# Kernel tuning notes

Measured on AMD Instinct MI355X. Metric: run time of the kernel, lower is better.

Reference implementation:

```python
import jax, jax.numpy as jnp
import numpy as np

B, T, IDIM = 16, 1024, 345
L, D, H, DK, FF = 4, 256, 4, 64, 1024
EPS = 1e-5


def layer_norm(x, s, b):
    m = jnp.mean(x, axis=-1, keepdims=True)
    v = jnp.mean(jnp.square(x - m), axis=-1, keepdims=True)
    return (x - m) * jax.lax.rsqrt(v + EPS) * s + b


def setup_inputs() -> dict:
    key = jax.random.key(0)
    ks = jax.random.split(key, 16)
    w = 0.02
    return {
        "x": jax.random.normal(ks[0], (B, T, IDIM), jnp.float32),
        "num_frames": int(T),
        "Win": w * jax.random.normal(ks[1], (IDIM, D), jnp.float32),
        "b_in": jnp.zeros((D,), jnp.float32),
        "ln1_s": jnp.ones((L, D), jnp.float32),
        "ln1_b": jnp.zeros((L, D), jnp.float32),
        "Wq": w * jax.random.normal(ks[2], (L, D, D), jnp.float32),
        "bq": jnp.zeros((L, D), jnp.float32),
        "Wk": w * jax.random.normal(ks[3], (L, D, D), jnp.float32),
        "bk": jnp.zeros((L, D), jnp.float32),
        "Wv": w * jax.random.normal(ks[4], (L, D, D), jnp.float32),
        "bv": jnp.zeros((L, D), jnp.float32),
        "Wo": w * jax.random.normal(ks[5], (L, D, D), jnp.float32),
        "bo": jnp.zeros((L, D), jnp.float32),
        "ln2_s": jnp.ones((L, D), jnp.float32),
        "ln2_b": jnp.zeros((L, D), jnp.float32),
        "W1": w * jax.random.normal(ks[6], (L, D, FF), jnp.float32),
        "b1": jnp.zeros((L, FF), jnp.float32),
        "W2": w * jax.random.normal(ks[7], (L, FF, D), jnp.float32),
        "b2": jnp.zeros((L, D), jnp.float32),
        "lno_s": jnp.ones((D,), jnp.float32),
        "lno_b": jnp.zeros((D,), jnp.float32),
    }


def reference(x, num_frames, Win, b_in, ln1_s, ln1_b, Wq, bq, Wk, bk, Wv, bv,
              Wo, bo, ln2_s, ln2_b, W1, b1, W2, b2, lno_s, lno_b):
    num = x.shape[0]
    scale = 1.0 / np.sqrt(DK)
    # [num*T, D]
    e = x.reshape(-1, x.shape[-1]) @ Win + b_in
    for i in range(L):
        e = layer_norm(e, ln1_s[i], ln1_b[i])
        # naive MHSA (residual taken from LN output, as in the source)
        q = (e @ Wq[i] + bq[i]).reshape(num, -1, H, DK)
        k = (e @ Wk[i] + bk[i]).reshape(num, -1, H, DK)
        v = (e @ Wv[i] + bv[i]).reshape(num, -1, H, DK)
        scores = jnp.einsum('bqhd,bkhd->bhqk', q, k) * scale
        attn = jax.nn.softmax(scores, axis=-1)
        o = jnp.einsum('bhqk,bkhd->bqhd', attn, v).reshape(-1, D)
        e = e + (o @ Wo[i] + bo[i])
        e = layer_norm(e, ln2_s[i], ln2_b[i])
        e = e + (jax.nn.relu(e @ W1[i] + b1[i]) @ W2[i] + b2[i])
    out = layer_norm(e, lno_s, lno_b)
    return out.reshape(num, num_frames, -1)
```

## Files before the change

kernel.cpp:

```cpp
#include <hip/hip_runtime.h>
#include <hip/hip_bf16.h>

#define BB    16
#define TT    1024
#define MTOK  (BB*TT)
#define IDIM_ 345
#define KPAD  384
#define LL    4
#define DD_   256
#define FF_   1024
#define EPS_  1e-5f
#define QSCL  0.18033688f
#define MSHIFT 12.0f

typedef __bf16 bf16;
typedef bf16 bf16x8 __attribute__((ext_vector_type(8)));
typedef float f32x4 __attribute__((ext_vector_type(4)));

static __device__ __forceinline__ f32x4 MFMA(bf16x8 a, bf16x8 b, f32x4 c) {
  return __builtin_amdgcn_mfma_f32_16x16x32_bf16(a, b, c, 0, 0, 0);
}
static __device__ __forceinline__ unsigned bfbits(float x) {
  return (unsigned)__builtin_bit_cast(unsigned short, (bf16)x);
}
static __device__ __forceinline__ bf16x8 ld_bf8(const void* p) {
  return *reinterpret_cast<const bf16x8*>(p);
}
static __device__ __forceinline__ void gload_lds16(const bf16* g, void* l) {
  __builtin_amdgcn_global_load_lds(
      (const __attribute__((address_space(1))) void*)g,
      (__attribute__((address_space(3))) void*)l, 16, 0, 0);
}

__global__ void k_convert_pad(const float* __restrict__ src, bf16* __restrict__ dst) {
  int idx = blockIdx.x * 256 + threadIdx.x;
  if (idx >= MTOK * (KPAD / 4)) return;
  int r = idx / (KPAD / 4), c0 = (idx % (KPAD / 4)) * 4;
  const float* s = src + (long)r * IDIM_ + c0;
  float v0 = (c0 + 0 < IDIM_) ? s[0] : 0.f;
  float v1 = (c0 + 1 < IDIM_) ? s[1] : 0.f;
  float v2 = (c0 + 2 < IDIM_) ? s[2] : 0.f;
  float v3 = (c0 + 3 < IDIM_) ? s[3] : 0.f;
  uint2 pk;
  pk.x = bfbits(v0) | (bfbits(v1) << 16);
  pk.y = bfbits(v2) | (bfbits(v3) << 16);
  *reinterpret_cast<uint2*>(dst + (long)r * KPAD + c0) = pk;
}

__global__ void k_wt_convert(const float* __restrict__ src, bf16* __restrict__ dst,
                             int K, int N, int Kp) {
  int idx = blockIdx.x * 256 + threadIdx.x;
  if (idx >= N * Kp) return;
  int n = idx / Kp, kk = idx % Kp;
  dst[idx] = (kk < K) ? (bf16)src[(long)kk * N + n] : (bf16)0.f;
}

__global__ __launch_bounds__(256)
void k_wt_all(const float* __restrict__ Wq, const float* __restrict__ Wk,
              const float* __restrict__ Wv, const float* __restrict__ Wo,
              const float* __restrict__ W1, const float* __restrict__ W2,
              bf16* __restrict__ Wqkvt, bf16* __restrict__ Wot,
              bf16* __restrict__ W1t, bf16* __restrict__ W2t) {
  __shared__ float tile[64][65];
  const int s = blockIdx.y, m = s >> 2, i = s & 3;
  const float* src; bf16* dst; int K, N;
  switch (m) {
    case 0: src = Wq + (long)i*65536;  dst = Wqkvt + (long)i*196608;          K=256;  N=256;  break;
    case 1: src = Wk + (long)i*65536;  dst = Wqkvt + (long)i*196608 + 65536;  K=256;  N=256;  break;
    case 2: src = Wv + (long)i*65536;  dst = Wqkvt + (long)i*196608 + 131072; K=256;  N=256;  break;
    case 3: src = Wo + (long)i*65536;  dst = Wot + (long)i*65536;             K=256;  N=256;  break;
    case 4: src = W1 + (long)i*262144; dst = W1t + (long)i*262144;            K=256;  N=1024; break;
    default:src = W2 + (long)i*262144; dst = W2t + (long)i*262144;            K=1024; N=256;  break;
  }
  const int tiles_n = N >> 6, ntiles = (K >> 6) * tiles_n;
  if (blockIdx.x >= ntiles) return;
  const int tk = blockIdx.x / tiles_n, tn = blockIdx.x % tiles_n;
  const int t = threadIdx.x, rq = t >> 6, cl = t & 63;
  #pragma unroll
  for (int i2 = 0; i2 < 16; i2++)
    tile[rq * 16 + i2][cl] = src[(long)(tk * 64 + rq * 16 + i2) * N + tn * 64 + cl];
  __syncthreads();
  #pragma unroll
  for (int i2 = 0; i2 < 16; i2++)
    dst[(long)(tn * 64 + rq * 16 + i2) * K + tk * 64 + cl] = (bf16)tile[cl][rq * 16 + i2];
}

__global__ void k_bias_concat(const float* __restrict__ bq, const float* __restrict__ bk,
                              const float* __restrict__ bv, float* __restrict__ bqkv) {
  int idx = blockIdx.x * 256 + threadIdx.x;
  if (idx >= LL * 768) return;
  int i = idx / 768, j = idx % 768;
  float v = (j < 256) ? bq[i*256 + j] : (j < 512 ? bk[i*256 + j - 256] : bv[i*256 + j - 512]);
  bqkv[idx] = v;
}

template<int EPI>
__global__ __launch_bounds__(512, 4)
void k_gemm_row(const bf16* __restrict__ A, const bf16* __restrict__ Wt,
                const float* __restrict__ bias, const bf16* __restrict__ resid,
                const float* __restrict__ lns, const float* __restrict__ lnb,
                void* __restrict__ out, int K) {
  __shared__ alignas(16) char As[4096];
  __shared__ alignas(16) char Bs[32768];
  __shared__ alignas(16) float redS[32][4];
  __shared__ alignas(16) float redQ[32][4];
  const int t = threadIdx.x, lane = t & 63, wid = t >> 6;
  const int wr = wid >> 2, wc = wid & 3;
  const int g = lane >> 4, c = lane & 15;
  int flat = blockIdx.x;
  flat = (flat & 7) * 64 + (flat >> 3);
  const int mbase = flat * 32;

  const int srow = t >> 3;
  const int slot = ((t & 7) ^ (srow & 7)) * 8;
  const bf16* ag = A  + (long)(mbase + srow) * K + slot;
  const bf16* bg = Wt + (long)srow * K + slot;
  const int swz = (c & 7) << 4;

  f32x4 acc[4] = {};

  const int nk = K >> 6;
  for (int kt = 0; kt < nk; ++kt) {
    const int k0 = kt * 64;
    __syncthreads();
    if (wid < 4) gload_lds16(ag + k0, As + wid * 1024);
    #pragma unroll
    for (int p = 0; p < 4; p++)
      gload_lds16(bg + (long)(p * 64) * K + k0, Bs + p * 8192 + wid * 1024);
    __syncthreads();

    bf16x8 af[2], bfr[4][2];
    #pragma unroll
    for (int ks = 0; ks < 2; ks++)
      af[ks] = ld_bf8(As + (wr * 16 + c) * 128 + ((ks * 64 + g * 16) ^ swz));
    #pragma unroll
    for (int ni = 0; ni < 4; ni++)
      #pragma unroll
      for (int ks = 0; ks < 2; ks++)
        bfr[ni][ks] = ld_bf8(Bs + (wc * 64 + ni * 16 + c) * 128 + ((ks * 64 + g * 16) ^ swz));
    __builtin_amdgcn_s_setprio(1);
    #pragma unroll
    for (int ni = 0; ni < 4; ni++)
      #pragma unroll
      for (int ks = 0; ks < 2; ks++)
        acc[ni] = MFMA(af[ks], bfr[ni][ks], acc[ni]);
    __builtin_amdgcn_s_setprio(0);
  }

  float v[4][4];
  float sP[4] = {0.f, 0.f, 0.f, 0.f}, qP[4] = {0.f, 0.f, 0.f, 0.f};
  #pragma unroll
  for (int ni = 0; ni < 4; ni++) {
    const int col = wc * 64 + ni * 16 + c;
    const float bb = bias[col];
    #pragma unroll
    for (int j = 0; j < 4; j++) {
      const int row = mbase + wr * 16 + g * 4 + j;
      float r = resid ? (float)resid[(long)row * 256 + col] : 0.f;
      float x = acc[ni][j] + bb + r;
      v[ni][j] = x;
      sP[j] += x;
      qP[j] += x * x;
    }
  }
  #pragma unroll
  for (int j = 0; j < 4; j++) {
    #pragma unroll
    for (int off = 1; off < 16; off <<= 1) {
      sP[j] += __shfl_xor(sP[j], off);
      qP[j] += __shfl_xor(qP[j], off);
    }
  }
  if (c == 0) {
    #pragma unroll
    for (int j = 0; j < 4; j++) {
      const int rb = wr * 16 + g * 4 + j;
      redS[rb][wc] = sP[j];
      redQ[rb][wc] = qP[j];
    }
  }
  __syncthreads();

  #pragma unroll
  for (int j = 0; j < 4; j++) {
    const int rb = wr * 16 + g * 4 + j;
    const float4 s4 = *reinterpret_cast<const float4*>(redS[rb]);
    const float4 q4 = *reinterpret_cast<const float4*>(redQ[rb]);
    const float mean = (s4.x + s4.y + s4.z + s4.w) * (1.f / 256.f);
    const float var = (q4.x + q4.y + q4.z + q4.w) * (1.f / 256.f) - mean * mean;
    const float rstd = rsqrtf(var + EPS_);
    const long row = mbase + wr * 16 + g * 4 + j;
    #pragma unroll
    for (int ni = 0; ni < 4; ni++) {
      const int col = wc * 64 + ni * 16 + c;
      const float y = (v[ni][j] - mean) * rstd * lns[col] + lnb[col];
      if constexpr (EPI == 0) {
        ((bf16*)out)[row * 256 + col] = (bf16)y;
      } else {
        ((float*)out)[row * 256 + col] = y;
      }
    }
  }
}

template<int EPI>
__global__ __launch_bounds__(512, 4)
void k_ffn(const bf16* __restrict__ e, const bf16* __restrict__ W1t,
           const float* __restrict__ b1, const bf16* __restrict__ W2t,
           const float* __restrict__ b2, const float* __restrict__ lns,
           const float* __restrict__ lnb, void* __restrict__ out) {
  __shared__ alignas(16) char Ae[16384];
  __shared__ alignas(16) char Hs[16384];
  __shared__ alignas(16) char Bs[32768];
  __shared__ alignas(16) float redS[32][4];
  __shared__ alignas(16) float redQ[32][4];
  const int t = threadIdx.x, lane = t & 63, wid = t >> 6;
  const int wr = wid >> 2, wc = wid & 3;
  const int g = lane >> 4, c = lane & 15;
  int flat = blockIdx.x;
  flat = (flat & 7) * 64 + (flat >> 3);
  const int mbase = flat * 32;
  const int swz = (c & 7) << 4;

  #pragma unroll
  for (int p = 0; p < 2; p++) {
    const int ch = p * 512 + t;
    const int row = ch >> 5, s = ch & 31;
    const int srcb = (s >> 3) * 128 + (((s & 7) ^ (row & 7)) << 4);
    gload_lds16(e + (long)(mbase + row) * 256 + (srcb >> 1),
                Ae + p * 8192 + wid * 1024);
  }

  const int srow = t >> 3;
  const int slot = ((t & 7) ^ (srow & 7)) * 8;
  const int arow = wr * 16 + c;
  const int axo = (arow & 7) << 4;

  f32x4 acc2[4] = {};
  asm volatile("s_waitcnt vmcnt(0)" ::: "memory");
  __builtin_amdgcn_s_barrier();

  #pragma unroll 1
  for (int q = 0; q < 4; q++) {
    f32x4 acc1[4] = {};
    const bf16* bg1 = W1t + (long)(q * 256 + srow) * 256 + slot;
    for (int kt = 0; kt < 4; ++kt) {
      __syncthreads();
      #pragma unroll
      for (int p = 0; p < 4; p++)
        gload_lds16(bg1 + (long)(p * 64) * 256 + kt * 64, Bs + p * 8192 + wid * 1024);
      __syncthreads();
      bf16x8 af[2], bfr[4][2];
      #pragma unroll
      for (int ks = 0; ks < 2; ks++)
        af[ks] = ld_bf8(Ae + arow * 512 + ((kt * 128 + ks * 64 + g * 16) ^ axo));
      #pragma unroll
      for (int ni = 0; ni < 4; ni++)
        #pragma unroll
        for (int ks = 0; ks < 2; ks++)
          bfr[ni][ks] = ld_bf8(Bs + (wc * 64 + ni * 16 + c) * 128 + ((ks * 64 + g * 16) ^ swz));
      __builtin_amdgcn_s_setprio(1);
      #pragma unroll
      for (int ni = 0; ni < 4; ni++)
        #pragma unroll
        for (int ks = 0; ks < 2; ks++)
          acc1[ni] = MFMA(af[ks], bfr[ni][ks], acc1[ni]);
      __builtin_amdgcn_s_setprio(0);
    }
    #pragma unroll
    for (int ni = 0; ni < 4; ni++) {
      const int col = wc * 64 + ni * 16 + c;
      const float bb = b1[q * 256 + col];
      #pragma unroll
      for (int j = 0; j < 4; j++) {
        const int row = wr * 16 + g * 4 + j;
        *(bf16*)(Hs + row * 512 + ((col * 2) ^ ((row & 7) << 4))) =
            (bf16)fmaxf(acc1[ni][j] + bb, 0.f);
      }
    }
    __syncthreads();
    const bf16* bg2 = W2t + (long)srow * 1024 + q * 256 + slot;
    for (int kt = 0; kt < 4; ++kt) {
      __syncthreads();
      #pragma unroll
      for (int p = 0; p < 4; p++)
        gload_lds16(bg2 + (long)(p * 64) * 1024 + kt * 64, Bs + p * 8192 + wid * 1024);
      __syncthreads();
      bf16x8 af[2], bfr[4][2];
      #pragma unroll
      for (int ks = 0; ks < 2; ks++)
        af[ks] = ld_bf8(Hs + arow * 512 + ((kt * 128 + ks * 64 + g * 16) ^ axo));
      #pragma unroll
      for (int ni = 0; ni < 4; ni++)
        #pragma unroll
        for (int ks = 0; ks < 2; ks++)
          bfr[ni][ks] = ld_bf8(Bs + (wc * 64 + ni * 16 + c) * 128 + ((ks * 64 + g * 16) ^ swz));
      __builtin_amdgcn_s_setprio(1);
      #pragma unroll
      for (int ni = 0; ni < 4; ni++)
        #pragma unroll
        for (int ks = 0; ks < 2; ks++)
          acc2[ni] = MFMA(af[ks], bfr[ni][ks], acc2[ni]);
      __builtin_amdgcn_s_setprio(0);
    }
  }

  float v[4][4];
  float sP[4] = {0.f, 0.f, 0.f, 0.f}, qP[4] = {0.f, 0.f, 0.f, 0.f};
  #pragma unroll
  for (int ni = 0; ni < 4; ni++) {
    const int col = wc * 64 + ni * 16 + c;
    const float bb = b2[col];
    #pragma unroll
    for (int j = 0; j < 4; j++) {
      const int row = wr * 16 + g * 4 + j;
      float r = (float)*(const bf16*)(Ae + row * 512 + ((col * 2) ^ ((row & 7) << 4)));
      float x = acc2[ni][j] + bb + r;
      v[ni][j] = x;
      sP[j] += x;
      qP[j] += x * x;
    }
  }
  #pragma unroll
  for (int j = 0; j < 4; j++) {
    #pragma unroll
    for (int off = 1; off < 16; off <<= 1) {
      sP[j] += __shfl_xor(sP[j], off);
      qP[j] += __shfl_xor(qP[j], off);
    }
  }
  if (c == 0) {
    #pragma unroll
    for (int j = 0; j < 4; j++) {
      const int rb = wr * 16 + g * 4 + j;
      redS[rb][wc] = sP[j];
      redQ[rb][wc] = qP[j];
    }
  }
  __syncthreads();

  #pragma unroll
  for (int j = 0; j < 4; j++) {
    const int rb = wr * 16 + g * 4 + j;
    const float4 s4 = *reinterpret_cast<const float4*>(redS[rb]);
    const float4 q4 = *reinterpret_cast<const float4*>(redQ[rb]);
    const float mean = (s4.x + s4.y + s4.z + s4.w) * (1.f / 256.f);
    const float var = (q4.x + q4.y + q4.z + q4.w) * (1.f / 256.f) - mean * mean;
    const float rstd = rsqrtf(var + EPS_);
    const long row = mbase + wr * 16 + g * 4 + j;
    #pragma unroll
    for (int ni = 0; ni < 4; ni++) {
      const int col = wc * 64 + ni * 16 + c;
      const float y = (v[ni][j] - mean) * rstd * lns[col] + lnb[col];
      if constexpr (EPI == 0) {
        ((bf16*)out)[row * 256 + col] = (bf16)y;
      } else {
        ((float*)out)[row * 256 + col] = y;
      }
    }
  }
}

template<int EPI>
__global__ __launch_bounds__(256)
void k_gemm_big(const bf16* __restrict__ A, const bf16* __restrict__ Wt,
                const float* __restrict__ bias, void* __restrict__ out,
                bf16* __restrict__ vt, int N, int K) {
  __shared__ alignas(16) char As[16384];
  __shared__ alignas(16) char Bs[16384];
  const int t = threadIdx.x, lane = t & 63, wid = t >> 6;
  const int wr = wid >> 1, wc = wid & 1;
  const int g = lane >> 4, c = lane & 15;
  int flat = blockIdx.y * gridDim.x + blockIdx.x;
  const int cpx = (gridDim.x * gridDim.y) >> 3;
  flat = (flat & 7) * cpx + (flat >> 3);
  const int mbase = (flat / gridDim.x) * 128, nbase = (flat % gridDim.x) * 128;

  const int srow = t >> 3;
  const int skc = ((t & 7) ^ (srow & 7)) * 8;
  const bf16* ag = A  + (long)(mbase + srow) * K + skc;
  const bf16* bg = Wt + (long)(nbase + srow) * K + skc;
  const int swz = (c & 7) << 4;

  f32x4 acc[4][4] = {};

  const int nk = K >> 6;
  for (int kt = 0; kt < nk; ++kt) {
    const int k0 = kt * 64;
    __syncthreads();
    #pragma unroll
    for (int p = 0; p < 4; p++) {
      gload_lds16(ag + (long)p * 32 * K + k0, As + p * 4096 + wid * 1024);
      gload_lds16(bg + (long)p * 32 * K + k0, Bs + p * 4096 + wid * 1024);
    }
    __syncthreads();

    bf16x8 af[4][2], bfr[4][2];
    #pragma unroll
    for (int mi = 0; mi < 4; mi++)
      #pragma unroll
      for (int ks = 0; ks < 2; ks++)
        af[mi][ks] = ld_bf8(As + (wr * 64 + mi * 16 + c) * 128 + ((ks * 64 + g * 16) ^ swz));
    #pragma unroll
    for (int ni = 0; ni < 4; ni++)
      #pragma unroll
      for (int ks = 0; ks < 2; ks++)
        bfr[ni][ks] = ld_bf8(Bs + (wc * 64 + ni * 16 + c) * 128 + ((ks * 64 + g * 16) ^ swz));
    __builtin_amdgcn_s_setprio(1);
    #pragma unroll
    for (int mi = 0; mi < 4; mi++)
      #pragma unroll
      for (int ni = 0; ni < 4; ni++)
        #pragma unroll
        for (int ks = 0; ks < 2; ks++)
          acc[mi][ni] = MFMA(af[mi][ks], bfr[ni][ks], acc[mi][ni]);
    __builtin_amdgcn_s_setprio(0);
  }

  #pragma unroll
  for (int mi = 0; mi < 4; mi++) {
    #pragma unroll
    for (int ni = 0; ni < 4; ni++) {
      const int colg = nbase + wc * 64 + ni * 16 + c;
      const float bv = bias ? bias[colg] : 0.f;
      if (nbase < 512) {
        const float qs = (nbase < 256) ? QSCL : 1.0f;
        #pragma unroll
        for (int j = 0; j < 4; j++) {
          const int rowg = mbase + wr * 64 + mi * 16 + g * 4 + j;
          ((bf16*)out)[(long)rowg * N + colg] = (bf16)((acc[mi][ni][j] + bv) * qs);
        }
      } else {
        const int dfull = colg - 512, hh = dfull >> 6, d = dfull & 63;
        const int rowg0 = mbase + wr * 64 + mi * 16 + g * 4;
        uint2 st;
        st.x = bfbits(acc[mi][ni][0] + bv) | (bfbits(acc[mi][ni][1] + bv) << 16);
        st.y = bfbits(acc[mi][ni][2] + bv) | (bfbits(acc[mi][ni][3] + bv) << 16);
        *reinterpret_cast<uint2*>(vt + (long)(((rowg0 >> 10) << 2) + hh) * 65536
                                     + d * 1024 + (rowg0 & 1023)) = st;
      }
    }
  }
}

__global__ __launch_bounds__(256)
void k_attn(const bf16* __restrict__ qkv, const bf16* __restrict__ vtg,
            bf16* __restrict__ o) {
  __shared__ alignas(16) char Ks[2][8192];
  __shared__ alignas(16) char Vs[2][8192];
  __shared__ alignas(16) char Ps[16384];
  const int t = threadIdx.x, lane = t & 63, w = t >> 6;
  const int g = lane >> 4, c = lane & 15;
  int flat = blockIdx.y * 8 + blockIdx.x;
  flat = (flat & 7) * 64 + (flat >> 3);
  const int bh = flat >> 3, qt = flat & 7;
  const int b = bh >> 2, h = bh & 3;
  const long tokbase = (long)b * TT;
  const int qA = qt * 128 + w * 16 + c;
  const int qB = qA + 64;

  bf16x8 qf0A = ld_bf8(qkv + (tokbase + qA) * 768 + h * 64 + g * 8);
  bf16x8 qf1A = ld_bf8(qkv + (tokbase + qA) * 768 + h * 64 + 32 + g * 8);
  bf16x8 qf0B = ld_bf8(qkv + (tokbase + qB) * 768 + h * 64 + g * 8);
  bf16x8 qf1B = ld_bf8(qkv + (tokbase + qB) * 768 + h * 64 + 32 + g * 8);

  const int sr = t >> 3;
  const int slot = (t & 7) ^ (sr & 7);
  const int swz_c = (c & 7) << 4;
  const bf16* kbase = qkv + 256 + h * 64 + slot * 8;
  const bf16* vbase = vtg + (long)bh * 65536 + slot * 8;
  char* pwA = Ps + w * 4096 + c * 128;
  char* pwB = pwA + 2048;

#define KSTAGE(bi, jt) do { \
    gload_lds16(kbase + (tokbase + (jt) * 64 + sr) * 768,      Ks[bi] + w * 1024); \
    gload_lds16(kbase + (tokbase + (jt) * 64 + sr + 32) * 768, Ks[bi] + 4096 + w * 1024); \
    gload_lds16(vbase + (long)sr * 1024 + (jt) * 64,           Vs[bi] + w * 1024); \
    gload_lds16(vbase + (long)(sr + 32) * 1024 + (jt) * 64,    Vs[bi] + 4096 + w * 1024); \
  } while (0)

  f32x4 oaccA[4] = {}, oaccB[4] = {};
  float lA = 0.f, lB = 0.f;

  KSTAGE(0, 0);
  int cur = 0;
  for (int jt = 0; jt < 16; ++jt) {
    if (jt + 1 < 16) {
      KSTAGE(cur ^ 1, jt + 1);
      asm volatile("s_waitcnt vmcnt(4)" ::: "memory");
    } else {
      asm volatile("s_waitcnt vmcnt(0)" ::: "memory");
    }
    __builtin_amdgcn_s_barrier();

    f32x4 saccA[4] = {}, saccB[4] = {};
    __builtin_amdgcn_s_setprio(1);
    #pragma unroll
    for (int ni = 0; ni < 4; ni++) {
      const char* krow = Ks[cur] + (ni * 16 + c) * 128;
      bf16x8 kf0 = ld_bf8(krow + ((g * 16) ^ swz_c));
      bf16x8 kf1 = ld_bf8(krow + ((64 + g * 16) ^ swz_c));
      saccA[ni] = MFMA(kf0, qf0A, saccA[ni]);
      saccB[ni] = MFMA(kf0, qf0B, saccB[ni]);
      saccA[ni] = MFMA(kf1, qf1A, saccA[ni]);
      saccB[ni] = MFMA(kf1, qf1B, saccB[ni]);
    }
    __builtin_amdgcn_s_setprio(0);

    #pragma unroll
    for (int ni = 0; ni < 4; ni++) {
      float a0 = __builtin_amdgcn_exp2f(saccA[ni][0] - MSHIFT);
      float b0 = __builtin_amdgcn_exp2f(saccB[ni][0] - MSHIFT);
      float a1 = __builtin_amdgcn_exp2f(saccA[ni][1] - MSHIFT);
      float b1 = __builtin_amdgcn_exp2f(saccB[ni][1] - MSHIFT);
      float a2 = __builtin_amdgcn_exp2f(saccA[ni][2] - MSHIFT);
      float b2 = __builtin_amdgcn_exp2f(saccB[ni][2] - MSHIFT);
      float a3 = __builtin_amdgcn_exp2f(saccA[ni][3] - MSHIFT);
      float b3 = __builtin_amdgcn_exp2f(saccB[ni][3] - MSHIFT);
      lA += (a0 + a1) + (a2 + a3);
      lB += (b0 + b1) + (b2 + b3);
      uint2 qa, qb;
      qa.x = bfbits(a0) | (bfbits(a1) << 16);
      qa.y = bfbits(a2) | (bfbits(a3) << 16);
      qb.x = bfbits(b0) | (bfbits(b1) << 16);
      qb.y = bfbits(b2) | (bfbits(b3) << 16);
      *reinterpret_cast<uint2*>(pwA + ((ni * 32 + g * 8) ^ swz_c)) = qa;
      *reinterpret_cast<uint2*>(pwB + ((ni * 32 + g * 8) ^ swz_c)) = qb;
    }

    __builtin_amdgcn_s_setprio(1);
    #pragma unroll
    for (int kk = 0; kk < 2; kk++) {
      bf16x8 pfA = ld_bf8(pwA + ((kk * 64 + g * 16) ^ swz_c));
      bf16x8 pfB = ld_bf8(pwB + ((kk * 64 + g * 16) ^ swz_c));
      #pragma unroll
      for (int nd = 0; nd < 4; nd++) {
        bf16x8 vf = ld_bf8(Vs[cur] + (nd * 16 + c) * 128 + ((kk * 64 + g * 16) ^ swz_c));
        oaccA[nd] = MFMA(vf, pfA, oaccA[nd]);
        oaccB[nd] = MFMA(vf, pfB, oaccB[nd]);
      }
    }
    __builtin_amdgcn_s_setprio(0);
    __builtin_amdgcn_s_barrier();
    cur ^= 1;
  }
#undef KSTAGE

  lA += __shfl_xor(lA, 16);
  lB += __shfl_xor(lB, 16);
  lA += __shfl_xor(lA, 32);
  lB += __shfl_xor(lB, 32);

  const float invA = 1.f / lA, invB = 1.f / lB;
  bf16* orowA = o + (tokbase + qA) * 256 + h * 64 + g * 4;
  bf16* orowB = o + (tokbase + qB) * 256 + h * 64 + g * 4;
  #pragma unroll
  for (int nd = 0; nd < 4; nd++) {
    uint2 sa, sb;
    sa.x = bfbits(oaccA[nd][0] * invA) | (bfbits(oaccA[nd][1] * invA) << 16);
    sa.y = bfbits(oaccA[nd][2] * invA) | (bfbits(oaccA[nd][3] * invA) << 16);
    sb.x = bfbits(oaccB[nd][0] * invB) | (bfbits(oaccB[nd][1] * invB) << 16);
    sb.y = bfbits(oaccB[nd][2] * invB) | (bfbits(oaccB[nd][3] * invB) << 16);
    *reinterpret_cast<uint2*>(orowA + nd * 16) = sa;
    *reinterpret_cast<uint2*>(orowB + nd * 16) = sb;
  }
}

extern "C" void kernel_launch(void* const* d_in, const int* in_sizes, int n_in,
                              void* d_out, int out_size, void* d_ws, size_t ws_size,
                              hipStream_t stream) {
  const float* x     = (const float*)d_in[0];
  const float* Win   = (const float*)d_in[2];
  const float* b_in  = (const float*)d_in[3];
  const float* ln1_s = (const float*)d_in[4];
  const float* ln1_b = (const float*)d_in[5];
  const float* Wq    = (const float*)d_in[6];
  const float* bq    = (const float*)d_in[7];
  const float* Wk    = (const float*)d_in[8];
  const float* bk    = (const float*)d_in[9];
  const float* Wv    = (const float*)d_in[10];
  const float* bv    = (const float*)d_in[11];
  const float* Wo    = (const float*)d_in[12];
  const float* bo    = (const float*)d_in[13];
  const float* ln2_s = (const float*)d_in[14];
  const float* ln2_b = (const float*)d_in[15];
  const float* W1    = (const float*)d_in[16];
  const float* b1    = (const float*)d_in[17];
  const float* W2    = (const float*)d_in[18];
  const float* b2    = (const float*)d_in[19];
  const float* lno_s = (const float*)d_in[20];
  const float* lno_b = (const float*)d_in[21];
  float* out = (float*)d_out;

  char* ws = (char*)d_ws;
  size_t off = 0;
  auto alloc = [&](size_t bytes) -> void* {
    void* p = ws + off; off += (bytes + 255) & ~(size_t)255; return p;
  };
  bf16* e_bf  = (bf16*)alloc((size_t)MTOK * DD_ * 2);
  bf16* qkvb  = (bf16*)alloc((size_t)MTOK * 768 * 2);
  bf16* vtb   = (bf16*)alloc((size_t)MTOK * DD_ * 2);
  bf16* ob    = (bf16*)alloc((size_t)MTOK * DD_ * 2);
  bf16* x_bf  = (bf16*)alloc((size_t)MTOK * KPAD * 2);
  bf16* Wint  = (bf16*)alloc((size_t)DD_ * KPAD * 2);
  bf16* Wqkvt = (bf16*)alloc((size_t)LL * 768 * DD_ * 2);
  bf16* Wot   = (bf16*)alloc((size_t)LL * DD_ * DD_ * 2);
  bf16* W1t   = (bf16*)alloc((size_t)LL * DD_ * FF_ * 2);
  bf16* W2t   = (bf16*)alloc((size_t)LL * FF_ * DD_ * 2);
  float* bqkv = (float*)alloc((size_t)LL * 768 * 4);

  dim3 blk(256);

  k_convert_pad<<<(MTOK * (KPAD / 4) + 255) / 256, 256, 0, stream>>>(x, x_bf);
  k_wt_convert<<<(DD_ * KPAD + 255) / 256, 256, 0, stream>>>(Win, Wint, IDIM_, DD_, KPAD);
  k_wt_all<<<dim3(64, 24), blk, 0, stream>>>(Wq, Wk, Wv, Wo, W1, W2, Wqkvt, Wot, W1t, W2t);
  k_bias_concat<<<(LL * 768 + 255) / 256, 256, 0, stream>>>(bq, bk, bv, bqkv);

  k_gemm_row<0><<<512, 512, 0, stream>>>(x_bf, Wint, b_in, nullptr,
                                         ln1_s, ln1_b, e_bf, KPAD);

  const long DDW = (long)DD_ * DD_;
  const long DFF = (long)DD_ * FF_;
  for (int i = 0; i < LL; i++) {
    k_gemm_big<3><<<dim3(6, 128), blk, 0, stream>>>(e_bf, Wqkvt + (long)i * 768 * DD_,
                                                    bqkv + i * 768, qkvb, vtb, 768, DD_);
    k_attn<<<dim3(8, 64), blk, 0, stream>>>(qkvb, vtb, ob);
    k_gemm_row<0><<<512, 512, 0, stream>>>(ob, Wot + i * DDW, bo + i * DD_, e_bf,
                                           ln2_s + i * DD_, ln2_b + i * DD_, e_bf, DD_);
    if (i < LL - 1) {
      k_ffn<0><<<512, 512, 0, stream>>>(e_bf, W1t + i * DFF, b1 + i * FF_,
                                        W2t + i * DFF, b2 + i * DD_,
                                        ln1_s + (i + 1) * DD_, ln1_b + (i + 1) * DD_, e_bf);
    } else {
      k_ffn<1><<<512, 512, 0, stream>>>(e_bf, W1t + i * DFF, b1 + i * FF_,
                                        W2t + i * DFF, b2 + i * DD_,
                                        lno_s, lno_b, out);
    }
  }
}
```

Measured before the change: 410.8 us.

## Halve attention query tile per block and split KV tiles across two accumulators

Each attention block now handles 64 queries instead of 128, and the grid doubles to 1024 blocks. Within a block the A/B accumulator pairs now cover two different KV tiles for the same queries rather than two query groups; the partial results are summed at the end. The double-buffered prefetch pipeline is replaced by a synchronous load of two KV tiles per iteration between barriers. This adds parallelism and cuts register use, but every K/V byte is now fetched twice as often across the grid and global-memory latency is no longer overlapped with compute.

Result: slower. 437.0 us (+6.4%).

```diff
diff --git a/kernel.cpp b/kernel.cpp
--- a/kernel.cpp
+++ b/kernel.cpp
@@ -451,18 +451,15 @@
   __shared__ alignas(16) char Ps[16384];
   const int t = threadIdx.x, lane = t & 63, w = t >> 6;
   const int g = lane >> 4, c = lane & 15;
-  int flat = blockIdx.y * 8 + blockIdx.x;
-  flat = (flat & 7) * 64 + (flat >> 3);
-  const int bh = flat >> 3, qt = flat & 7;
+  int flat = blockIdx.y * 16 + blockIdx.x;
+  flat = (flat & 7) * 128 + (flat >> 3);
+  const int bh = flat >> 4, qt = flat & 15;
   const int b = bh >> 2, h = bh & 3;
   const long tokbase = (long)b * TT;
-  const int qA = qt * 128 + w * 16 + c;
-  const int qB = qA + 64;
-
-  bf16x8 qf0A = ld_bf8(qkv + (tokbase + qA) * 768 + h * 64 + g * 8);
-  bf16x8 qf1A = ld_bf8(qkv + (tokbase + qA) * 768 + h * 64 + 32 + g * 8);
-  bf16x8 qf0B = ld_bf8(qkv + (tokbase + qB) * 768 + h * 64 + g * 8);
-  bf16x8 qf1B = ld_bf8(qkv + (tokbase + qB) * 768 + h * 64 + 32 + g * 8);
+  const int q_glob = qt * 64 + w * 16 + c;
+
+  bf16x8 qf0 = ld_bf8(qkv + (tokbase + q_glob) * 768 + h * 64 + g * 8);
+  bf16x8 qf1 = ld_bf8(qkv + (tokbase + q_glob) * 768 + h * 64 + 32 + g * 8);
 
   const int sr = t >> 3;
   const int slot = (t & 7) ^ (sr & 7);
@@ -472,38 +469,36 @@
   char* pwA = Ps + w * 4096 + c * 128;
   char* pwB = pwA + 2048;
 
-#define KSTAGE(bi, jt) do { \
-    gload_lds16(kbase + (tokbase + (jt) * 64 + sr) * 768,      Ks[bi] + w * 1024); \
-    gload_lds16(kbase + (tokbase + (jt) * 64 + sr + 32) * 768, Ks[bi] + 4096 + w * 1024); \
-    gload_lds16(vbase + (long)sr * 1024 + (jt) * 64,           Vs[bi] + w * 1024); \
-    gload_lds16(vbase + (long)(sr + 32) * 1024 + (jt) * 64,    Vs[bi] + 4096 + w * 1024); \
-  } while (0)
-
   f32x4 oaccA[4] = {}, oaccB[4] = {};
   float lA = 0.f, lB = 0.f;
 
-  KSTAGE(0, 0);
-  int cur = 0;
-  for (int jt = 0; jt < 16; ++jt) {
-    if (jt + 1 < 16) {
-      KSTAGE(cur ^ 1, jt + 1);
-      asm volatile("s_waitcnt vmcnt(4)" ::: "memory");
-    } else {
-      asm volatile("s_waitcnt vmcnt(0)" ::: "memory");
-    }
-    __builtin_amdgcn_s_barrier();
+  for (int jt = 0; jt < 8; ++jt) {
+    const int jA = 2 * jt, jB = 2 * jt + 1;
+    __syncthreads();
+    gload_lds16(kbase + (tokbase + jA * 64 + sr) * 768,      Ks[0] + w * 1024);
+    gload_lds16(kbase + (tokbase + jA * 64 + sr + 32) * 768, Ks[0] + 4096 + w * 1024);
+    gload_lds16(kbase + (tokbase + jB * 64 + sr) * 768,      Ks[1] + w * 1024);
+    gload_lds16(kbase + (tokbase + jB * 64 + sr + 32) * 768, Ks[1] + 4096 + w * 1024);
+    gload_lds16(vbase + (long)sr * 1024 + jA * 64,           Vs[0] + w * 1024);
+    gload_lds16(vbase + (long)(sr + 32) * 1024 + jA * 64,    Vs[0] + 4096 + w * 1024);
+    gload_lds16(vbase + (long)sr * 1024 + jB * 64,           Vs[1] + w * 1024);
+    gload_lds16(vbase + (long)(sr + 32) * 1024 + jB * 64,    Vs[1] + 4096 + w * 1024);
+    __syncthreads();
 
     f32x4 saccA[4] = {}, saccB[4] = {};
     __builtin_amdgcn_s_setprio(1);
     #pragma unroll
     for (int ni = 0; ni < 4; ni++) {
-      const char* krow = Ks[cur] + (ni * 16 + c) * 128;
-      bf16x8 kf0 = ld_bf8(krow + ((g * 16) ^ swz_c));
-      bf16x8 kf1 = ld_bf8(krow + ((64 + g * 16) ^ swz_c));
-      saccA[ni] = MFMA(kf0, qf0A, saccA[ni]);
-      saccB[ni] = MFMA(kf0, qf0B, saccB[ni]);
-      saccA[ni] = MFMA(kf1, qf1A, saccA[ni]);
-      saccB[ni] = MFMA(kf1, qf1B, saccB[ni]);
+      const char* krA = Ks[0] + (ni * 16 + c) * 128;
+      const char* krB = Ks[1] + (ni * 16 + c) * 128;
+      bf16x8 kfA0 = ld_bf8(krA + ((g * 16) ^ swz_c));
+      bf16x8 kfB0 = ld_bf8(krB + ((g * 16) ^ swz_c));
+      bf16x8 kfA1 = ld_bf8(krA + ((64 + g * 16) ^ swz_c));
+      bf16x8 kfB1 = ld_bf8(krB + ((64 + g * 16) ^ swz_c));
+      saccA[ni] = MFMA(kfA0, qf0, saccA[ni]);
+      saccB[ni] = MFMA(kfB0, qf0, saccB[ni]);
+      saccA[ni] = MFMA(kfA1, qf1, saccA[ni]);
+      saccB[ni] = MFMA(kfB1, qf1, saccB[ni]);
     }
     __builtin_amdgcn_s_setprio(0);
 
@@ -535,34 +530,28 @@
       bf16x8 pfB = ld_bf8(pwB + ((kk * 64 + g * 16) ^ swz_c));
       #pragma unroll
       for (int nd = 0; nd < 4; nd++) {
-        bf16x8 vf = ld_bf8(Vs[cur] + (nd * 16 + c) * 128 + ((kk * 64 + g * 16) ^ swz_c));
-        oaccA[nd] = MFMA(vf, pfA, oaccA[nd]);
-        oaccB[nd] = MFMA(vf, pfB, oaccB[nd]);
+        bf16x8 vfA = ld_bf8(Vs[0] + (nd * 16 + c) * 128 + ((kk * 64 + g * 16) ^ swz_c));
+        bf16x8 vfB = ld_bf8(Vs[1] + (nd * 16 + c) * 128 + ((kk * 64 + g * 16) ^ swz_c));
+        oaccA[nd] = MFMA(vfA, pfA, oaccA[nd]);
+        oaccB[nd] = MFMA(vfB, pfB, oaccB[nd]);
       }
     }
     __builtin_amdgcn_s_setprio(0);
-    __builtin_amdgcn_s_barrier();
-    cur ^= 1;
-  }
-#undef KSTAGE
-
-  lA += __shfl_xor(lA, 16);
-  lB += __shfl_xor(lB, 16);
-  lA += __shfl_xor(lA, 32);
-  lB += __shfl_xor(lB, 32);
-
-  const float invA = 1.f / lA, invB = 1.f / lB;
-  bf16* orowA = o + (tokbase + qA) * 256 + h * 64 + g * 4;
-  bf16* orowB = o + (tokbase + qB) * 256 + h * 64 + g * 4;
+  }
+
+  float l = lA + lB;
+  l += __shfl_xor(l, 16);
+  l += __shfl_xor(l, 32);
+  const float inv = 1.f / l;
+
+  bf16* orow = o + (tokbase + q_glob) * 256 + h * 64 + g * 4;
   #pragma unroll
   for (int nd = 0; nd < 4; nd++) {
-    uint2 sa, sb;
-    sa.x = bfbits(oaccA[nd][0] * invA) | (bfbits(oaccA[nd][1] * invA) << 16);
-    sa.y = bfbits(oaccA[nd][2] * invA) | (bfbits(oaccA[nd][3] * invA) << 16);
-    sb.x = bfbits(oaccB[nd][0] * invB) | (bfbits(oaccB[nd][1] * invB) << 16);
-    sb.y = bfbits(oaccB[nd][2] * invB) | (bfbits(oaccB[nd][3] * invB) << 16);
-    *reinterpret_cast<uint2*>(orowA + nd * 16) = sa;
-    *reinterpret_cast<uint2*>(orowB + nd * 16) = sb;
+    f32x4 om = oaccA[nd] + oaccB[nd];
+    uint2 st;
+    st.x = bfbits(om[0] * inv) | (bfbits(om[1] * inv) << 16);
+    st.y = bfbits(om[2] * inv) | (bfbits(om[3] * inv) << 16);
+    *reinterpret_cast<uint2*>(orow + nd * 16) = st;
   }
 }
 
@@ -624,7 +613,7 @@
   for (int i = 0; i < LL; i++) {
     k_gemm_big<3><<<dim3(6, 128), blk, 0, stream>>>(e_bf, Wqkvt + (long)i * 768 * DD_,
                                                     bqkv + i * 768, qkvb, vtb, 768, DD_);
-    k_attn<<<dim3(8, 64), blk, 0, stream>>>(qkvb, vtb, ob);
+    k_attn<<<dim3(16, 64), blk, 0, stream>>>(qkvb, vtb, ob);
     k_gemm_row<0><<<512, 512, 0, stream>>>(ob, Wot + i * DDW, bo + i * DD_, e_bf,
                                            ln2_s + i * DD_, ln2_b + i * DD_, e_bf, DD_);
     if (i < LL - 1) {
```

## Double-buffer FFN weight tiles and double rows per block

Applied to the files above, without the earlier changes.

The fused FFN kernel now handles 64 token rows per block instead of 32, so each loaded W1/W2 tile is reused across twice as many rows, and the grid shrinks to 256 blocks. Weight tiles are double-buffered in LDS, with the next stage's global-to-LDS load issued before computing the current one, replacing the two-syncthreads-per-step pattern with a single flattened 32-stage loop. LDS use rises to about 128KB per block and occupancy is lowered to 2 blocks per CU, while each wave holds twice the accumulators. This trades parallelism and register pressure for more reuse and more load/compute overlap.

Result: no change. 416.5 us (+1.4%).

```diff
diff --git a/kernel.cpp b/kernel.cpp
--- a/kernel.cpp
+++ b/kernel.cpp
@@ -204,26 +204,26 @@
 }
 
 template<int EPI>
-__global__ __launch_bounds__(512, 4)
+__global__ __launch_bounds__(512, 2)
 void k_ffn(const bf16* __restrict__ e, const bf16* __restrict__ W1t,
            const float* __restrict__ b1, const bf16* __restrict__ W2t,
            const float* __restrict__ b2, const float* __restrict__ lns,
            const float* __restrict__ lnb, void* __restrict__ out) {
-  __shared__ alignas(16) char Ae[16384];
-  __shared__ alignas(16) char Hs[16384];
-  __shared__ alignas(16) char Bs[32768];
-  __shared__ alignas(16) float redS[32][4];
-  __shared__ alignas(16) float redQ[32][4];
+  __shared__ alignas(16) char Ae[32768];
+  __shared__ alignas(16) char Hs[32768];
+  __shared__ alignas(16) char Bs[2][32768];
+  __shared__ alignas(16) float redS[64][4];
+  __shared__ alignas(16) float redQ[64][4];
   const int t = threadIdx.x, lane = t & 63, wid = t >> 6;
   const int wr = wid >> 2, wc = wid & 3;
   const int g = lane >> 4, c = lane & 15;
   int flat = blockIdx.x;
-  flat = (flat & 7) * 64 + (flat >> 3);
-  const int mbase = flat * 32;
+  flat = (flat & 7) * 32 + (flat >> 3);
+  const int mbase = flat * 64;
   const int swz = (c & 7) << 4;
 
   #pragma unroll
-  for (int p = 0; p < 2; p++) {
+  for (int p = 0; p < 4; p++) {
     const int ch = p * 512 + t;
     const int row = ch >> 5, s = ch & 31;
     const int srcb = (s >> 3) * 128 + (((s & 7) ^ (row & 7)) << 4);
@@ -233,129 +233,158 @@
 
   const int srow = t >> 3;
   const int slot = ((t & 7) ^ (srow & 7)) * 8;
-  const int arow = wr * 16 + c;
-  const int axo = (arow & 7) << 4;
-
-  f32x4 acc2[4] = {};
+
+  auto stage = [&](int s) {
+    const int q = s >> 3, ph = (s >> 2) & 1, kt = s & 3;
+    const bf16* bp;
+    long stride;
+    if (ph == 0) { bp = W1t + (long)(q * 256 + srow) * 256 + slot + kt * 64; stride = 256; }
+    else         { bp = W2t + (long)srow * 1024 + q * 256 + slot + kt * 64;  stride = 1024; }
+    #pragma unroll
+    for (int p = 0; p < 4; p++)
+      gload_lds16(bp + (long)(p * 64) * stride, Bs[s & 1] + p * 8192 + wid * 1024);
+  };
+
+  f32x4 acc1[2][4];
+  f32x4 acc2[2][4] = {};
+
+  stage(0);
   asm volatile("s_waitcnt vmcnt(0)" ::: "memory");
   __builtin_amdgcn_s_barrier();
 
-  #pragma unroll 1
-  for (int q = 0; q < 4; q++) {
-    f32x4 acc1[4] = {};
-    const bf16* bg1 = W1t + (long)(q * 256 + srow) * 256 + slot;
-    for (int kt = 0; kt < 4; ++kt) {
-      __syncthreads();
-      #pragma unroll
-      for (int p = 0; p < 4; p++)
-        gload_lds16(bg1 + (long)(p * 64) * 256 + kt * 64, Bs + p * 8192 + wid * 1024);
-      __syncthreads();
-      bf16x8 af[2], bfr[4][2];
+  for (int s = 0; s < 32; ++s) {
+    const int q = s >> 3, ph = (s >> 2) & 1, kt = s & 3;
+    if (s + 1 < 32) {
+      stage(s + 1);
+      asm volatile("s_waitcnt vmcnt(4)" ::: "memory");
+    } else {
+      asm volatile("s_waitcnt vmcnt(0)" ::: "memory");
+    }
+    __builtin_amdgcn_s_barrier();
+
+    if (ph == 0 && kt == 0) {
+      #pragma unroll
+      for (int mi = 0; mi < 2; mi++)
+        #pragma unroll
+        for (int ni = 0; ni < 4; ni++)
+          acc1[mi][ni] = f32x4{0.f, 0.f, 0.f, 0.f};
+    }
+
+    const char* Asrc = (ph == 0) ? Ae : Hs;
+    bf16x8 af[2][2], bfr[4][2];
+    #pragma unroll
+    for (int mi = 0; mi < 2; mi++) {
+      const int arow = wr * 32 + mi * 16 + c;
+      const int axo = (arow & 7) << 4;
       #pragma unroll
       for (int ks = 0; ks < 2; ks++)
-        af[ks] = ld_bf8(Ae + arow * 512 + ((kt * 128 + ks * 64 + g * 16) ^ axo));
-      #pragma unroll
-      for (int ni = 0; ni < 4; ni++)
+        af[mi][ks] = ld_bf8(Asrc + arow * 512 + ((kt * 128 + ks * 64 + g * 16) ^ axo));
+    }
+    #pragma unroll
+    for (int ni = 0; ni < 4; ni++)
+      #pragma unroll
+      for (int ks = 0; ks < 2; ks++)
+        bfr[ni][ks] = ld_bf8(Bs[s & 1] + (wc * 64 + ni * 16 + c) * 128 + ((ks * 64 + g * 16) ^ swz));
+    __builtin_amdgcn_s_setprio(1);
+    if (ph == 0) {
+      #pragma unroll
+      for (int mi = 0; mi < 2; mi++)
         #pragma unroll
-        for (int ks = 0; ks < 2; ks++)
-          bfr[ni][ks] = ld_bf8(Bs + (wc * 64 + ni * 16 + c) * 128 + ((ks * 64 + g * 16) ^ swz));
-      __builtin_amdgcn_s_setprio(1);
-      #pragma unroll
-      for (int ni = 0; ni < 4; ni++)
+        for (int ni = 0; ni < 4; ni++)
+          #pragma unroll
+          for (int ks = 0; ks < 2; ks++)
+            acc1[mi][ni] = MFMA(af[mi][ks], bfr[ni][ks], acc1[mi][ni]);
+    } else {
+      #pragma unroll
+      for (int mi = 0; mi < 2; mi++)
         #pragma unroll
-        for (int ks = 0; ks < 2; ks++)
-          acc1[ni] = MFMA(af[ks], bfr[ni][ks], acc1[ni]);
-      __builtin_amdgcn_s_setprio(0);
-    }
+        for (int ni = 0; ni < 4; ni++)
+          #pragma unroll
+          for (int ks = 0; ks < 2; ks++)
+            acc2[mi][ni] = MFMA(af[mi][ks], bfr[ni][ks], acc2[mi][ni]);
+    }
+    __builtin_amdgcn_s_setprio(0);
+
+    if (ph == 0 && kt == 3) {
+      #pragma unroll
+      for (int mi = 0; mi < 2; mi++)
+        #pragma unroll
+        for (int ni = 0; ni < 4; ni++) {
+          const int col = wc * 64 + ni * 16 + c;
+          const float bb = b1[q * 256 + col];
+          #pragma unroll
+          for (int j = 0; j < 4; j++) {
+            const int row = wr * 32 + mi * 16 + g * 4 + j;
+            *(bf16*)(Hs + row * 512 + ((col * 2) ^ ((row & 7) << 4))) =
+                (bf16)fmaxf(acc1[mi][ni][j] + bb, 0.f);
+          }
+        }
+    }
+    asm volatile("s_waitcnt lgkmcnt(0)" ::: "memory");
+    __builtin_amdgcn_s_barrier();
+  }
+
+  float v[2][4][4];
+  float sP[2][4] = {}, qP[2][4] = {};
+  #pragma unroll
+  for (int mi = 0; mi < 2; mi++) {
     #pragma unroll
     for (int ni = 0; ni < 4; ni++) {
       const int col = wc * 64 + ni * 16 + c;
-      const float bb = b1[q * 256 + col];
+      const float bb = b2[col];
       #pragma unroll
       for (int j = 0; j < 4; j++) {
-        const int row = wr * 16 + g * 4 + j;
-        *(bf16*)(Hs + row * 512 + ((col * 2) ^ ((row & 7) << 4))) =
-            (bf16)fmaxf(acc1[ni][j] + bb, 0.f);
+        const int row = wr * 32 + mi * 16 + g * 4 + j;
+        float r = (float)*(const bf16*)(Ae + row * 512 + ((col * 2) ^ ((row & 7) << 4)));
+        float x = acc2[mi][ni][j] + bb + r;
+        v[mi][ni][j] = x;
+        sP[mi][j] += x;
+        qP[mi][j] += x * x;
       }
     }
-    __syncthreads();
-    const bf16* bg2 = W2t + (long)srow * 1024 + q * 256 + slot;
-    for (int kt = 0; kt < 4; ++kt) {
-      __syncthreads();
-      #pragma unroll
-      for (int p = 0; p < 4; p++)
-        gload_lds16(bg2 + (long)(p * 64) * 1024 + kt * 64, Bs + p * 8192 + wid * 1024);
-      __syncthreads();
-      bf16x8 af[2], bfr[4][2];
-      #pragma unroll
-      for (int ks = 0; ks < 2; ks++)
-        af[ks] = ld_bf8(Hs + arow * 512 + ((kt * 128 + ks * 64 + g * 16) ^ axo));
-      #pragma unroll
-      for (int ni = 0; ni < 4; ni++)
-        #pragma unroll
-        for (int ks = 0; ks < 2; ks++)
-          bfr[ni][ks] = ld_bf8(Bs + (wc * 64 + ni * 16 + c) * 128 + ((ks * 64 + g * 16) ^ swz));
-      __builtin_amdgcn_s_setprio(1);
-      #pragma unroll
-      for (int ni = 0; ni < 4; ni++)
-        #pragma unroll
-        for (int ks = 0; ks < 2; ks++)
-          acc2[ni] = MFMA(af[ks], bfr[ni][ks], acc2[ni]);
-      __builtin_amdgcn_s_setprio(0);
-    }
-  }
-
-  float v[4][4];
-  float sP[4] = {0.f, 0.f, 0.f, 0.f}, qP[4] = {0.f, 0.f, 0.f, 0.f};
-  #pragma unroll
-  for (int ni = 0; ni < 4; ni++) {
-    const int col = wc * 64 + ni * 16 + c;
-    const float bb = b2[col];
+  }
+  #pragma unroll
+  for (int mi = 0; mi < 2; mi++)
     #pragma unroll
     for (int j = 0; j < 4; j++) {
-      const int row = wr * 16 + g * 4 + j;
-      float r = (float)*(const bf16*)(Ae + row * 512 + ((col * 2) ^ ((row & 7) << 4)));
-      float x = acc2[ni][j] + bb + r;
-      v[ni][j] = x;
-      sP[j] += x;
-      qP[j] += x * x;
-    }
-  }
-  #pragma unroll
-  for (int j = 0; j < 4; j++) {
-    #pragma unroll
-    for (int off = 1; off < 16; off <<= 1) {
-      sP[j] += __shfl_xor(sP[j], off);
-      qP[j] += __shfl_xor(qP[j], off);
-    }
-  }
+      #pragma unroll
+      for (int off = 1; off < 16; off <<= 1) {
+        sP[mi][j] += __shfl_xor(sP[mi][j], off);
+        qP[mi][j] += __shfl_xor(qP[mi][j], off);
+      }
+    }
   if (c == 0) {
     #pragma unroll
+    for (int mi = 0; mi < 2; mi++)
+      #pragma unroll
+      for (int j = 0; j < 4; j++) {
+        const int rb = wr * 32 + mi * 16 + g * 4 + j;
+        redS[rb][wc] = sP[mi][j];
+        redQ[rb][wc] = qP[mi][j];
+      }
+  }
+  __syncthreads();
+
+  #pragma unroll
+  for (int mi = 0; mi < 2; mi++) {
+    #pragma unroll
     for (int j = 0; j < 4; j++) {
-      const int rb = wr * 16 + g * 4 + j;
-      redS[rb][wc] = sP[j];
-      redQ[rb][wc] = qP[j];
-    }
-  }
-  __syncthreads();
-
-  #pragma unroll
-  for (int j = 0; j < 4; j++) {
-    const int rb = wr * 16 + g * 4 + j;
-    const float4 s4 = *reinterpret_cast<const float4*>(redS[rb]);
-    const float4 q4 = *reinterpret_cast<const float4*>(redQ[rb]);
-    const float mean = (s4.x + s4.y + s4.z + s4.w) * (1.f / 256.f);
-    const float var = (q4.x + q4.y + q4.z + q4.w) * (1.f / 256.f) - mean * mean;
-    const float rstd = rsqrtf(var + EPS_);
-    const long row = mbase + wr * 16 + g * 4 + j;
-    #pragma unroll
-    for (int ni = 0; ni < 4; ni++) {
-      const int col = wc * 64 + ni * 16 + c;
-      const float y = (v[ni][j] - mean) * rstd * lns[col] + lnb[col];
-      if constexpr (EPI == 0) {
-        ((bf16*)out)[row * 256 + col] = (bf16)y;
-      } else {
-        ((float*)out)[row * 256 + col] = y;
+      const int rb = wr * 32 + mi * 16 + g * 4 + j;
+      const float4 s4 = *reinterpret_cast<const float4*>(redS[rb]);
+      const float4 q4 = *reinterpret_cast<const float4*>(redQ[rb]);
+      const float mean = (s4.x + s4.y + s4.z + s4.w) * (1.f / 256.f);
+      const float var = (q4.x + q4.y + q4.z + q4.w) * (1.f / 256.f) - mean * mean;
+      const float rstd = rsqrtf(var + EPS_);
+      const long row = mbase + rb;
+      #pragma unroll
+      for (int ni = 0; ni < 4; ni++) {
+        const int col = wc * 64 + ni * 16 + c;
+        const float y = (v[mi][ni][j] - mean) * rstd * lns[col] + lnb[col];
+        if constexpr (EPI == 0) {
+          ((bf16*)out)[row * 256 + col] = (bf16)y;
+        } else {
+          ((float*)out)[row * 256 + col] = y;
+        }
       }
     }
   }
@@ -628,11 +657,11 @@
     k_gemm_row<0><<<512, 512, 0, stream>>>(ob, Wot + i * DDW, bo + i * DD_, e_bf,
                                            ln2_s + i * DD_, ln2_b + i * DD_, e_bf, DD_);
     if (i < LL - 1) {
-      k_ffn<0><<<512, 512, 0, stream>>>(e_bf, W1t + i * DFF, b1 + i * FF_,
+      k_ffn<0><<<256, 512, 0, stream>>>(e_bf, W1t + i * DFF, b1 + i * FF_,
                                         W2t + i * DFF, b2 + i * DD_,
                                         ln1_s + (i + 1) * DD_, ln1_b + (i + 1) * DD_, e_bf);
     } else {
-      k_ffn<1><<<512, 512, 0, stream>>>(e_bf, W1t + i * DFF, b1 + i * FF_,
+      k_ffn<1><<<256, 512, 0, stream>>>(e_bf, W1t + i * DFF, b1 + i * FF_,
                                         W2t + i * DFF, b2 + i * DD_,
                                         lno_s, lno_b, out);
     }
```
